# Kernel tuning notes

Measured on AMD Instinct MI355X. Metric: run time of the kernel, lower is better.

The kernel has to match this reference:

```python
import jax, jax.numpy as jnp
import numpy as np

D_MODEL = 1024
NUM_HEADS = 16
HDIM = D_MODEL // NUM_HEADS
THETA = 10000.0


def setup_inputs() -> dict:
    key = jax.random.key(0)
    ks = jax.random.split(key, 5)
    bs, seq = 4, 2048
    std = np.sqrt(2.0 / (D_MODEL + D_MODEL))
    def w(k):
        # trunc_normal approximated by clipped normal (same distribution family)
        return jnp.clip(std * jax.random.normal(k, (D_MODEL, D_MODEL), jnp.float32), -3 * std, 3 * std)
    return {
        "x": jax.random.normal(ks[0], (bs, seq, D_MODEL), jnp.float32),
        "Wq": w(ks[1]), "Wk": w(ks[2]), "Wv": w(ks[3]), "Wo": w(ks[4]),
        "token_positions": jnp.arange(seq, dtype=jnp.int64),
    }


def _rope(x, token_positions):
    # x: (bs, H, S, hdim); rotate even/odd interleaved pairs
    inv_freq = THETA ** (-2.0 * jnp.arange(HDIM // 2, dtype=jnp.float32) / HDIM)
    freqs = token_positions.astype(jnp.float32)[:, None] * inv_freq[None, :]  # (S, hdim/2)
    cos, sin = jnp.cos(freqs), jnp.sin(freqs)
    x_even, x_odd = x[..., 0::2], x[..., 1::2]
    out_even = x_even * cos - x_odd * sin
    out_odd = x_odd * cos + x_even * sin
    # interleave back: stack on new last axis then reshape
    return jnp.stack([out_even, out_odd], axis=-1).reshape(x.shape)


def reference(x, Wq, Wk, Wv, Wo, token_positions):
    bs, seq, _ = x.shape
    q = (x @ Wq.T).reshape(bs, seq, NUM_HEADS, HDIM).transpose(0, 2, 1, 3)
    k = (x @ Wk.T).reshape(bs, seq, NUM_HEADS, HDIM).transpose(0, 2, 1, 3)
    v = (x @ Wv.T).reshape(bs, seq, NUM_HEADS, HDIM).transpose(0, 2, 1, 3)
    q = _rope(q, token_positions)
    k = _rope(k, token_positions)
    scores = jnp.einsum("bhsd,bhtd->bhst", q, k) / jnp.sqrt(jnp.float32(HDIM))
    mask = jnp.tril(jnp.ones((seq, seq), dtype=bool))
    scores = jnp.where(mask, scores, -jnp.inf)
    attn = jax.nn.softmax(scores, axis=-1)
    out = jnp.einsum("bhst,bhtd->bhsd", attn, v)
    out = out.transpose(0, 2, 1, 3).reshape(bs, seq, D_MODEL)
    return out @ Wo.T
```

## Files before the change

### kernel.cpp

```cpp
#include <hip/hip_runtime.h>
#include <hip/hip_fp16.h>

typedef _Float16 half8 __attribute__((ext_vector_type(8)));
typedef _Float16 half4 __attribute__((ext_vector_type(4)));
typedef _Float16 half2v __attribute__((ext_vector_type(2)));
typedef float f32x4 __attribute__((ext_vector_type(4)));

#define SEQ   2048
#define DM    1024
#define NH    16
#define HD    64
#define BSZ   4

#if __has_builtin(__builtin_amdgcn_exp2f)
#define EXP2(x) __builtin_amdgcn_exp2f(x)
#else
#define EXP2(x) exp2f(x)
#endif

#define QSCALE 0.1803368801f

__device__ __forceinline__ void gload16(const void* g, void* l) {
  __builtin_amdgcn_global_load_lds((const __attribute__((address_space(1))) void*)g,
                                   (__attribute__((address_space(3))) void*)l,
                                   16, 0, 0);
}

__device__ __forceinline__ f32x4 vmax4(f32x4 a, f32x4 b) {
  f32x4 r;
  r[0] = fmaxf(a[0], b[0]); r[1] = fmaxf(a[1], b[1]);
  r[2] = fmaxf(a[2], b[2]); r[3] = fmaxf(a[3], b[3]);
  return r;
}

__global__ void cvt4(const float* __restrict__ src, _Float16* __restrict__ dst, int n4) {
  int i = blockIdx.x * blockDim.x + threadIdx.x;
  if (i < n4) {
    float4 v = ((const float4*)src)[i];
    half4 o = { (_Float16)v.x, (_Float16)v.y, (_Float16)v.z, (_Float16)v.w };
    ((half4*)dst)[i] = o;
  }
}

template<int MODE>
__global__ __launch_bounds__(256)
void gemm_hk(const _Float16* __restrict__ A, const _Float16* __restrict__ B,
             _Float16* __restrict__ oQ, _Float16* __restrict__ oK,
             _Float16* __restrict__ oVt, float* __restrict__ oF) {
  __shared__ _Float16 As[128*32];
  __shared__ _Float16 Bs[128*32];
  const int tid  = threadIdx.x;
  const int wid  = tid >> 6, lane = tid & 63;
  const int wm   = wid >> 1, wn = wid & 1;
  const int fr   = lane & 15, fg = lane >> 4;
  const long m0  = (long)blockIdx.x * 128;
  const long n0  = (long)blockIdx.y * 128;
  const int lrow = lane >> 2;
  const int lcol = (lane & 3) * 8;
  const _Float16* ga0 = A + (m0 + wid*32 + lrow) * 1024 + lcol;
  const _Float16* gb0 = B + (n0 + wid*32 + lrow) * 1024 + lcol;
  _Float16* lA = &As[wid*32*32];
  _Float16* lB = &Bs[wid*32*32];

  f32x4 acc[4][4] = {};

  for (int k0 = 0; k0 < 1024; k0 += 32) {
    gload16(ga0 + k0,             lA);
    gload16(ga0 + k0 + 16*1024,   lA + 16*32);
    gload16(gb0 + k0,             lB);
    gload16(gb0 + k0 + 16*1024,   lB + 16*32);
    __syncthreads();
    half8 af[4], bf[4];
#pragma unroll
    for (int i = 0; i < 4; ++i) {
      af[i] = *(const half8*)&As[(wm*64 + i*16 + fr)*32 + fg*8];
      bf[i] = *(const half8*)&Bs[(wn*64 + i*16 + fr)*32 + fg*8];
    }
#pragma unroll
    for (int i = 0; i < 4; ++i)
#pragma unroll
      for (int j = 0; j < 4; ++j)
        acc[i][j] = __builtin_amdgcn_mfma_f32_16x16x32_f16(af[i], bf[j], acc[i][j], 0, 0, 0);
    __syncthreads();
  }

  if (MODE == 0) {
    const int which = (int)(n0 >> 10);
    const int nloc0 = ((int)n0 & 1023) + wn*64;
#pragma unroll
    for (int i = 0; i < 4; ++i) {
      const long r0 = m0 + wm*64 + i*16 + fg*4;
      const int  bb = (int)(r0 >> 11);
      const int  s  = (int)(r0 & 2047);
#pragma unroll
      for (int j = 0; j < 4; ++j) {
        const int nl = nloc0 + j*16 + fr;
        const int h  = nl >> 6, d = nl & 63;
        const long bh = (long)(bb*NH + h);
        if (which == 0) {
#pragma unroll
          for (int r = 0; r < 4; ++r)
            oQ[(bh*SEQ + s + r)*HD + d] = (_Float16)(acc[i][j][r] * QSCALE);
        } else if (which == 1) {
#pragma unroll
          for (int r = 0; r < 4; ++r)
            oK[(bh*SEQ + s + r)*HD + d] = (_Float16)acc[i][j][r];
        } else {
          half4 pk = { (_Float16)acc[i][j][0], (_Float16)acc[i][j][1],
                       (_Float16)acc[i][j][2], (_Float16)acc[i][j][3] };
          *(half4*)&oVt[(bh*HD + d)*SEQ + s] = pk;
        }
      }
    }
  } else {
#pragma unroll
    for (int i = 0; i < 4; ++i) {
      const long r0 = m0 + wm*64 + i*16 + fg*4;
#pragma unroll
      for (int j = 0; j < 4; ++j) {
        const long col = n0 + wn*64 + j*16 + fr;
#pragma unroll
        for (int r = 0; r < 4; ++r)
          oF[(r0 + r)*DM + col] = acc[i][j][r];
      }
    }
  }
}

__global__ void rope_k(_Float16* __restrict__ Q, _Float16* __restrict__ K,
                       const int* __restrict__ tp) {
  const int t = blockIdx.x * blockDim.x + threadIdx.x;
  const int s = t >> 5, p = t & 31;
  _Float16* base = blockIdx.z ? K : Q;
  half2v* ptr = (half2v*)(base + ((long)blockIdx.y * SEQ + s) * HD) + p;
  half2v v = *ptr;
  const float pos = (float)tp[s];
  const float inv = exp2f(-0.41524101186f * (float)p);
  const float f = pos * inv;
  float sn, cs;
  __sincosf(f, &sn, &cs);
  const float xe = (float)v[0], xo = (float)v[1];
  half2v o = { (_Float16)(xe*cs - xo*sn), (_Float16)(xo*cs + xe*sn) };
  *ptr = o;
}

__global__ __launch_bounds__(256, 4)
void fattn(const _Float16* __restrict__ Q, const _Float16* __restrict__ K,
           const _Float16* __restrict__ Vt, _Float16* __restrict__ O) {
  __shared__ _Float16 Ks[2][64*64];
  __shared__ _Float16 Vs[2][64*64];
  __shared__ _Float16 Ps[4][16*64];
  const int tid = threadIdx.x, wid = tid >> 6, lane = tid & 63;
  const int fr = lane & 15, fg = lane >> 4;
  const int bh = blockIdx.x;
  const int b = bh >> 4, h = bh & 15;
  const int y = blockIdx.y;
  const int q0H = (31 - y) * 64;
  const int q0L = y * 64;
  const int qs_[2] = { q0H + wid*16, q0L + wid*16 };
  const _Float16* Qb = Q + (long)bh * SEQ * HD;
  const _Float16* Kb = K + (long)bh * SEQ * HD;
  const _Float16* Vb = Vt + (long)bh * HD * SEQ;

  half8 qf[2][2];
#pragma unroll
  for (int s = 0; s < 2; ++s) {
    qf[s][0] = *(const half8*)&Qb[(qs_[s] + fr)*HD + fg*8];
    qf[s][1] = *(const half8*)&Qb[(qs_[s] + fr)*HD + 32 + fg*8];
  }

  f32x4 oaccT[2][4] = {};
  float m_s[2] = { -1e30f, -1e30f }, l_s[2] = { 0.f, 0.f };

  const int srow = lane >> 3;
  const int sc16 = (lane & 7) ^ srow;
  const int r1 = wid*16 + srow, r2 = r1 + 8;

  char* Pb = (char*)&Ps[wid][0];
  const int swp = (fr & 7) << 4;
  const int nt = (q0H >> 6) + 1;

  gload16(Kb + (long)r1*HD + sc16*8, &Ks[0][(wid*16)*64]);
  gload16(Kb + (long)r2*HD + sc16*8, &Ks[0][(wid*16 + 8)*64]);
  gload16(Vb + (long)r1*SEQ + sc16*8, &Vs[0][(wid*16)*64]);
  gload16(Vb + (long)r2*SEQ + sc16*8, &Vs[0][(wid*16 + 8)*64]);
  __syncthreads();

  int cur = 0;
  for (int t = 0; t < nt; ++t) {
    const int kv0 = t * 64;

    if (t + 1 < nt) {
      const int nkv = kv0 + 64;
      gload16(Kb + (long)(nkv + r1)*HD + sc16*8, &Ks[cur^1][(wid*16)*64]);
      gload16(Kb + (long)(nkv + r2)*HD + sc16*8, &Ks[cur^1][(wid*16 + 8)*64]);
      gload16(Vb + (long)r1*SEQ + nkv + sc16*8,  &Vs[cur^1][(wid*16)*64]);
      gload16(Vb + (long)r2*SEQ + nkv + sc16*8,  &Vs[cur^1][(wid*16 + 8)*64]);
    }

    const char* Kc = (const char*)&Ks[cur][0];
    const char* Vc = (const char*)&Vs[cur][0];

#pragma unroll
    for (int s = 0; s < 2; ++s) {
      const int qs0 = qs_[s];
      if (kv0 > qs0 + 15) continue;
      const int qa = qs0 + fr;

      f32x4 sa[4];
      __builtin_amdgcn_s_setprio(1);
#pragma unroll
      for (int n = 0; n < 4; ++n) {
        const int row = n*16 + fr;
        const int sw = (row & 7) << 4;
        const half8 k0v = *(const half8*)(Kc + row*128 + ((fg*16) ^ sw));
        const half8 k1v = *(const half8*)(Kc + row*128 + ((64 + fg*16) ^ sw));
        f32x4 z = {0.f, 0.f, 0.f, 0.f};
        z = __builtin_amdgcn_mfma_f32_16x16x32_f16(k0v, qf[s][0], z, 0, 0, 0);
        sa[n] = __builtin_amdgcn_mfma_f32_16x16x32_f16(k1v, qf[s][1], z, 0, 0, 0);
      }
      __builtin_amdgcn_s_setprio(0);

      if (kv0 + 63 > qs0) {
#pragma unroll
        for (int n = 0; n < 4; ++n) {
          const int kvb = kv0 + n*16 + fg*4;
#pragma unroll
          for (int r = 0; r < 4; ++r)
            if (kvb + r > qa) sa[n][r] = -1e30f;
        }
      }

      f32x4 mx = vmax4(vmax4(sa[0], sa[1]), vmax4(sa[2], sa[3]));
      float pm = fmaxf(fmaxf(mx[0], mx[1]), fmaxf(mx[2], mx[3]));
      pm = fmaxf(pm, __shfl_xor(pm, 16));
      pm = fmaxf(pm, __shfl_xor(pm, 32));

      if (!__all(pm <= m_s[s] + 8.0f)) {
        const float mn = fmaxf(m_s[s], pm);
        const float fac = EXP2(m_s[s] - mn);
        m_s[s] = mn;
        l_s[s] *= fac;
#pragma unroll
        for (int n = 0; n < 4; ++n) oaccT[s][n] *= fac;
      }
      const float mrow = m_s[s];

#pragma unroll
      for (int n = 0; n < 4; ++n)
#pragma unroll
        for (int r = 0; r < 4; ++r)
          sa[n][r] = EXP2(sa[n][r] - mrow);

      f32x4 s4 = (sa[0] + sa[1]) + (sa[2] + sa[3]);
      float ps = (s4[0] + s4[1]) + (s4[2] + s4[3]);
      ps += __shfl_xor(ps, 16);
      ps += __shfl_xor(ps, 32);
      l_s[s] += ps;

#pragma unroll
      for (int n = 0; n < 4; ++n) {
        half2v lo = (half2v)__builtin_amdgcn_cvt_pkrtz(sa[n][0], sa[n][1]);
        half2v hi = (half2v)__builtin_amdgcn_cvt_pkrtz(sa[n][2], sa[n][3]);
        half4 p4 = __builtin_shufflevector(lo, hi, 0, 1, 2, 3);
        *(half4*)(Pb + ((fr*128 + n*32 + fg*8) ^ swp)) = p4;
      }

      __builtin_amdgcn_s_setprio(1);
#pragma unroll
      for (int ks = 0; ks < 2; ++ks) {
        const half8 pf = *(const half8*)(Pb + ((fr*128 + ks*64 + fg*16) ^ swp));
#pragma unroll
        for (int nd = 0; nd < 4; ++nd) {
          const int row = nd*16 + fr;
          const int sw = (row & 7) << 4;
          const half8 vf = *(const half8*)(Vc + row*128 + ((ks*64 + fg*16) ^ sw));
          oaccT[s][nd] = __builtin_amdgcn_mfma_f32_16x16x32_f16(vf, pf, oaccT[s][nd], 0, 0, 0);
        }
      }
      __builtin_amdgcn_s_setprio(0);
    }

    __syncthreads();
    cur ^= 1;
  }

#pragma unroll
  for (int s = 0; s < 2; ++s) {
    const float rl = __builtin_amdgcn_rcpf(l_s[s]);
    _Float16* orow = O + ((long)b*SEQ + (qs_[s] + fr))*DM + h*64;
#pragma unroll
    for (int nd = 0; nd < 4; ++nd) {
      half2v lo = (half2v)__builtin_amdgcn_cvt_pkrtz(oaccT[s][nd][0]*rl, oaccT[s][nd][1]*rl);
      half2v hi = (half2v)__builtin_amdgcn_cvt_pkrtz(oaccT[s][nd][2]*rl, oaccT[s][nd][3]*rl);
      half4 o4 = __builtin_shufflevector(lo, hi, 0, 1, 2, 3);
      *(half4*)&orow[nd*16 + fg*4] = o4;
    }
  }
}

extern "C" void kernel_launch(void* const* d_in, const int* in_sizes, int n_in,
                              void* d_out, int out_size, void* d_ws, size_t ws_size,
                              hipStream_t stream) {
  const float* x  = (const float*)d_in[0];
  const float* Wq = (const float*)d_in[1];
  const float* Wk = (const float*)d_in[2];
  const float* Wv = (const float*)d_in[3];
  const float* Wo = (const float*)d_in[4];
  const int*   tp = (const int*)d_in[5];
  float* out = (float*)d_out;

  char* ws = (char*)d_ws;
  _Float16* xh   = (_Float16*)(ws);
  _Float16* Wqkv = (_Float16*)(ws + (16u << 20));
  _Float16* Woh  = (_Float16*)(ws + (22u << 20));
  _Float16* Qb   = (_Float16*)(ws + (24u << 20));
  _Float16* Kb   = (_Float16*)(ws + (40u << 20));
  _Float16* Vtb  = (_Float16*)(ws + (56u << 20));
  _Float16* attn = (_Float16*)(ws + (72u << 20));

  cvt4<<<8192, 256, 0, stream>>>(x,  xh, 2097152);
  cvt4<<<1024, 256, 0, stream>>>(Wq, Wqkv,               262144);
  cvt4<<<1024, 256, 0, stream>>>(Wk, Wqkv + (1u << 20),  262144);
  cvt4<<<1024, 256, 0, stream>>>(Wv, Wqkv + (2u << 20),  262144);
  cvt4<<<1024, 256, 0, stream>>>(Wo, Woh,                262144);

  gemm_hk<0><<<dim3(64, 24), 256, 0, stream>>>(xh, Wqkv, Qb, Kb, Vtb, nullptr);
  rope_k<<<dim3(256, 64, 2), 256, 0, stream>>>(Qb, Kb, tp);
  fattn<<<dim3(64, 16), 256, 0, stream>>>(Qb, Kb, Vtb, attn);
  gemm_hk<1><<<dim3(64, 8), 256, 0, stream>>>(attn, Woh, nullptr, nullptr, nullptr, out);
}
```

Baseline: 195.1 us.

## Switch flash attention to 32x32x16 MFMA with 32-row query tiles per wave

Rewrites the attention kernel so each wave handles 32 query rows using 32x32x16 MFMA instructions instead of 16x16x32. Each block now covers two 128-row query chunks (paired heavy and light causal halves), which halves the grid. Each 64-wide KV tile is processed in two 32-column halves. The larger tile raises K/V reuse per LDS read and cuts the shuffle reductions, but it uses more registers per thread (occupancy hint drops from 4 to 3) and launches fewer blocks, which weakens load balancing.

```diff
diff --git a/kernel.cpp b/kernel.cpp
--- a/kernel.cpp
+++ b/kernel.cpp
@@ -5,6 +5,8 @@
 typedef _Float16 half4 __attribute__((ext_vector_type(4)));
 typedef _Float16 half2v __attribute__((ext_vector_type(2)));
 typedef float f32x4 __attribute__((ext_vector_type(4)));
+typedef float f32x8v __attribute__((ext_vector_type(8)));
+typedef float f32x16 __attribute__((ext_vector_type(16)));
 
 #define SEQ   2048
 #define DM    1024
@@ -24,13 +26,6 @@
   __builtin_amdgcn_global_load_lds((const __attribute__((address_space(1))) void*)g,
                                    (__attribute__((address_space(3))) void*)l,
                                    16, 0, 0);
-}
-
-__device__ __forceinline__ f32x4 vmax4(f32x4 a, f32x4 b) {
-  f32x4 r;
-  r[0] = fmaxf(a[0], b[0]); r[1] = fmaxf(a[1], b[1]);
-  r[2] = fmaxf(a[2], b[2]); r[3] = fmaxf(a[3], b[3]);
-  return r;
 }
 
 __global__ void cvt4(const float* __restrict__ src, _Float16* __restrict__ dst, int n4) {
@@ -144,32 +139,29 @@
   *ptr = o;
 }
 
-__global__ __launch_bounds__(256, 4)
+__global__ __launch_bounds__(256, 3)
 void fattn(const _Float16* __restrict__ Q, const _Float16* __restrict__ K,
            const _Float16* __restrict__ Vt, _Float16* __restrict__ O) {
   __shared__ _Float16 Ks[2][64*64];
   __shared__ _Float16 Vs[2][64*64];
-  __shared__ _Float16 Ps[4][16*64];
+  __shared__ _Float16 Ps[4][32*32];
   const int tid = threadIdx.x, wid = tid >> 6, lane = tid & 63;
-  const int fr = lane & 15, fg = lane >> 4;
-  const int bh = blockIdx.x;
-  const int b = bh >> 4, h = bh & 15;
+  const int q31 = lane & 31, hi = lane >> 5;
+  const int bh = blockIdx.x, b = bh >> 4, h = bh & 15;
   const int y = blockIdx.y;
-  const int q0H = (31 - y) * 64;
-  const int q0L = y * 64;
-  const int qs_[2] = { q0H + wid*16, q0L + wid*16 };
+  const int qs_[2] = { (15 - y)*128 + wid*32, y*128 + wid*32 };
   const _Float16* Qb = Q + (long)bh * SEQ * HD;
   const _Float16* Kb = K + (long)bh * SEQ * HD;
   const _Float16* Vb = Vt + (long)bh * HD * SEQ;
 
-  half8 qf[2][2];
-#pragma unroll
-  for (int s = 0; s < 2; ++s) {
-    qf[s][0] = *(const half8*)&Qb[(qs_[s] + fr)*HD + fg*8];
-    qf[s][1] = *(const half8*)&Qb[(qs_[s] + fr)*HD + 32 + fg*8];
-  }
-
-  f32x4 oaccT[2][4] = {};
+  half8 qf[2][4];
+#pragma unroll
+  for (int s = 0; s < 2; ++s)
+#pragma unroll
+    for (int c = 0; c < 4; ++c)
+      qf[s][c] = *(const half8*)&Qb[(qs_[s] + q31)*HD + c*16 + hi*8];
+
+  f32x16 oacc[2][2] = {};
   float m_s[2] = { -1e30f, -1e30f }, l_s[2] = { 0.f, 0.f };
 
   const int srow = lane >> 3;
@@ -177,8 +169,8 @@
   const int r1 = wid*16 + srow, r2 = r1 + 8;
 
   char* Pb = (char*)&Ps[wid][0];
-  const int swp = (fr & 7) << 4;
-  const int nt = (q0H >> 6) + 1;
+  const int swp = (q31 & 3) << 4;
+  const int nt = (15 - y)*2 + 2;
 
   gload16(Kb + (long)r1*HD + sc16*8, &Ks[0][(wid*16)*64]);
   gload16(Kb + (long)r2*HD + sc16*8, &Ks[0][(wid*16 + 8)*64]);
@@ -202,83 +194,86 @@
     const char* Vc = (const char*)&Vs[cur][0];
 
 #pragma unroll
-    for (int s = 0; s < 2; ++s) {
-      const int qs0 = qs_[s];
-      if (kv0 > qs0 + 15) continue;
-      const int qa = qs0 + fr;
-
-      f32x4 sa[4];
-      __builtin_amdgcn_s_setprio(1);
-#pragma unroll
-      for (int n = 0; n < 4; ++n) {
-        const int row = n*16 + fr;
-        const int sw = (row & 7) << 4;
-        const half8 k0v = *(const half8*)(Kc + row*128 + ((fg*16) ^ sw));
-        const half8 k1v = *(const half8*)(Kc + row*128 + ((64 + fg*16) ^ sw));
-        f32x4 z = {0.f, 0.f, 0.f, 0.f};
-        z = __builtin_amdgcn_mfma_f32_16x16x32_f16(k0v, qf[s][0], z, 0, 0, 0);
-        sa[n] = __builtin_amdgcn_mfma_f32_16x16x32_f16(k1v, qf[s][1], z, 0, 0, 0);
+    for (int hh = 0; hh < 2; ++hh) {
+      const int kvb = kv0 + 32*hh;
+#pragma unroll
+      for (int s = 0; s < 2; ++s) {
+        const int qs0 = qs_[s];
+        if (kvb > qs0 + 31) continue;
+
+        f32x16 sa = {};
+        __builtin_amdgcn_s_setprio(1);
+#pragma unroll
+        for (int c = 0; c < 4; ++c) {
+          const int row = 32*hh + q31;
+          const half8 kf = *(const half8*)(Kc + row*128 + ((c*32 + hi*16) ^ ((row & 7) << 4)));
+          sa = __builtin_amdgcn_mfma_f32_32x32x16_f16(kf, qf[s][c], sa, 0, 0, 0);
+        }
+        __builtin_amdgcn_s_setprio(0);
+
+        if (kvb + 31 > qs0) {
+          const int thr = qs0 + q31 - kvb - 4*hi;
+#pragma unroll
+          for (int r = 0; r < 16; ++r) {
+            const int cr = (r & 3) + 8*(r >> 2);
+            if (cr > thr) sa[r] = -1e30f;
+          }
+        }
+
+        f32x8v mx8;
+#pragma unroll
+        for (int i = 0; i < 8; ++i) mx8[i] = fmaxf(sa[i], sa[i+8]);
+        f32x4 mx4;
+#pragma unroll
+        for (int i = 0; i < 4; ++i) mx4[i] = fmaxf(mx8[i], mx8[i+4]);
+        float pm = fmaxf(fmaxf(mx4[0], mx4[1]), fmaxf(mx4[2], mx4[3]));
+        pm = fmaxf(pm, __shfl_xor(pm, 32));
+
+        if (!__all(pm <= m_s[s] + 8.0f)) {
+          const float mn = fmaxf(m_s[s], pm);
+          const float fac = EXP2(m_s[s] - mn);
+          m_s[s] = mn;
+          l_s[s] *= fac;
+          oacc[s][0] *= fac;
+          oacc[s][1] *= fac;
+        }
+        const float mrow = m_s[s];
+
+#pragma unroll
+        for (int r = 0; r < 16; ++r) sa[r] = EXP2(sa[r] - mrow);
+
+        f32x8v s8;
+#pragma unroll
+        for (int i = 0; i < 8; ++i) s8[i] = sa[i] + sa[i+8];
+        f32x4 s4v;
+#pragma unroll
+        for (int i = 0; i < 4; ++i) s4v[i] = s8[i] + s8[i+4];
+        float ps = (s4v[0] + s4v[1]) + (s4v[2] + s4v[3]);
+        ps += __shfl_xor(ps, 32);
+        l_s[s] += ps;
+
+#pragma unroll
+        for (int g = 0; g < 4; ++g) {
+          half2v lo  = (half2v)__builtin_amdgcn_cvt_pkrtz(sa[4*g+0], sa[4*g+1]);
+          half2v hi2 = (half2v)__builtin_amdgcn_cvt_pkrtz(sa[4*g+2], sa[4*g+3]);
+          half4 p4 = __builtin_shufflevector(lo, hi2, 0, 1, 2, 3);
+          *(half4*)(Pb + q31*64 + ((g*16 + hi*8) ^ swp)) = p4;
+        }
+
+        __builtin_amdgcn_s_setprio(1);
+#pragma unroll
+        for (int ks = 0; ks < 2; ++ks) {
+          const half8 pf = *(const half8*)(Pb + q31*64 + ((ks*32 + hi*16) ^ swp));
+#pragma unroll
+          for (int nd = 0; nd < 2; ++nd) {
+            const int row = nd*32 + q31;
+            const half8 vf = *(const half8*)(Vc + row*128 +
+                              ((hh*64 + ks*32 + hi*16) ^ ((row & 7) << 4)));
+            oacc[s][nd] = __builtin_amdgcn_mfma_f32_32x32x16_f16(vf, pf, oacc[s][nd], 0, 0, 0);
+          }
+        }
+        __builtin_amdgcn_s_setprio(0);
       }
-      __builtin_amdgcn_s_setprio(0);
-
-      if (kv0 + 63 > qs0) {
-#pragma unroll
-        for (int n = 0; n < 4; ++n) {
-          const int kvb = kv0 + n*16 + fg*4;
-#pragma unroll
-          for (int r = 0; r < 4; ++r)
-            if (kvb + r > qa) sa[n][r] = -1e30f;
-        }
-      }
-
-      f32x4 mx = vmax4(vmax4(sa[0], sa[1]), vmax4(sa[2], sa[3]));
-      float pm = fmaxf(fmaxf(mx[0], mx[1]), fmaxf(mx[2], mx[3]));
-      pm = fmaxf(pm, __shfl_xor(pm, 16));
-      pm = fmaxf(pm, __shfl_xor(pm, 32));
-
-      if (!__all(pm <= m_s[s] + 8.0f)) {
-        const float mn = fmaxf(m_s[s], pm);
-        const float fac = EXP2(m_s[s] - mn);
-        m_s[s] = mn;
-        l_s[s] *= fac;
-#pragma unroll
-        for (int n = 0; n < 4; ++n) oaccT[s][n] *= fac;
-      }
-      const float mrow = m_s[s];
-
-#pragma unroll
-      for (int n = 0; n < 4; ++n)
-#pragma unroll
-        for (int r = 0; r < 4; ++r)
-          sa[n][r] = EXP2(sa[n][r] - mrow);
-
-      f32x4 s4 = (sa[0] + sa[1]) + (sa[2] + sa[3]);
-      float ps = (s4[0] + s4[1]) + (s4[2] + s4[3]);
-      ps += __shfl_xor(ps, 16);
-      ps += __shfl_xor(ps, 32);
-      l_s[s] += ps;
-
-#pragma unroll
-      for (int n = 0; n < 4; ++n) {
-        half2v lo = (half2v)__builtin_amdgcn_cvt_pkrtz(sa[n][0], sa[n][1]);
-        half2v hi = (half2v)__builtin_amdgcn_cvt_pkrtz(sa[n][2], sa[n][3]);
-        half4 p4 = __builtin_shufflevector(lo, hi, 0, 1, 2, 3);
-        *(half4*)(Pb + ((fr*128 + n*32 + fg*8) ^ swp)) = p4;
-      }
-
-      __builtin_amdgcn_s_setprio(1);
-#pragma unroll
-      for (int ks = 0; ks < 2; ++ks) {
-        const half8 pf = *(const half8*)(Pb + ((fr*128 + ks*64 + fg*16) ^ swp));
-#pragma unroll
-        for (int nd = 0; nd < 4; ++nd) {
-          const int row = nd*16 + fr;
-          const int sw = (row & 7) << 4;
-          const half8 vf = *(const half8*)(Vc + row*128 + ((ks*64 + fg*16) ^ sw));
-          oaccT[s][nd] = __builtin_amdgcn_mfma_f32_16x16x32_f16(vf, pf, oaccT[s][nd], 0, 0, 0);
-        }
-      }
-      __builtin_amdgcn_s_setprio(0);
     }
 
     __syncthreads();
@@ -288,14 +283,16 @@
 #pragma unroll
   for (int s = 0; s < 2; ++s) {
     const float rl = __builtin_amdgcn_rcpf(l_s[s]);
-    _Float16* orow = O + ((long)b*SEQ + (qs_[s] + fr))*DM + h*64;
-#pragma unroll
-    for (int nd = 0; nd < 4; ++nd) {
-      half2v lo = (half2v)__builtin_amdgcn_cvt_pkrtz(oaccT[s][nd][0]*rl, oaccT[s][nd][1]*rl);
-      half2v hi = (half2v)__builtin_amdgcn_cvt_pkrtz(oaccT[s][nd][2]*rl, oaccT[s][nd][3]*rl);
-      half4 o4 = __builtin_shufflevector(lo, hi, 0, 1, 2, 3);
-      *(half4*)&orow[nd*16 + fg*4] = o4;
-    }
+    _Float16* orow = O + ((long)b*SEQ + (qs_[s] + q31))*DM + h*64;
+#pragma unroll
+    for (int nd = 0; nd < 2; ++nd)
+#pragma unroll
+      for (int g = 0; g < 4; ++g) {
+        half2v lo  = (half2v)__builtin_amdgcn_cvt_pkrtz(oacc[s][nd][4*g+0]*rl, oacc[s][nd][4*g+1]*rl);
+        half2v hi2 = (half2v)__builtin_amdgcn_cvt_pkrtz(oacc[s][nd][4*g+2]*rl, oacc[s][nd][4*g+3]*rl);
+        half4 o4 = __builtin_shufflevector(lo, hi2, 0, 1, 2, 3);
+        *(half4*)&orow[nd*32 + g*8 + 4*hi] = o4;
+      }
   }
 }
 
@@ -327,6 +324,6 @@
 
   gemm_hk<0><<<dim3(64, 24), 256, 0, stream>>>(xh, Wqkv, Qb, Kb, Vtb, nullptr);
   rope_k<<<dim3(256, 64, 2), 256, 0, stream>>>(Qb, Kb, tp);
-  fattn<<<dim3(64, 16), 256, 0, stream>>>(Qb, Kb, Vtb, attn);
+  fattn<<<dim3(64, 8), 256, 0, stream>>>(Qb, Kb, Vtb, attn);
   gemm_hk<1><<<dim3(64, 8), 256, 0, stream>>>(attn, Woh, nullptr, nullptr, nullptr, out);
 }
```

After: 201.9 us. +3.5%, slower.
